# Kernel optimization log

Measured on AMD Instinct MI355X. Metric: run time of the kernel, lower is better.

The kernel has to match this reference:

```python
import jax, jax.numpy as jnp
import numpy as np

EPS = 1e-05  # matches tf entropy epsilon


def setup_inputs() -> dict:
    key = jax.random.key(0)
    k1, k2 = jax.random.split(key)
    encodings = jax.random.normal(k1, (8192, 64), dtype=jnp.float32)
    categorical = jax.random.uniform(k2, (8192, 25), dtype=jnp.float32)
    return {"encodings": encodings, "categorical": categorical, "k": 15}


def reference(encodings, categorical, k):
    B = encodings.shape[0]
    n_components = categorical.shape[1]
    k = min(k, B // 4)  # layer clamps k to batch_size // 4

    hard_groups = jnp.argmax(categorical, axis=1)           # [B] int
    max_groups = jnp.max(categorical, axis=1)               # [B]

    # Batched brute-force kNN. tf.norm's sqrt is monotonic, so the strict
    # comparison `dist < kth_dist` is identical on squared distances; working
    # in squared space avoids sqrt(0) issues and an extra pass.
    sq = jnp.sum(encodings * encodings, axis=1)             # [B]
    d2 = sq[:, None] + sq[None, :] - 2.0 * (encodings @ encodings.T)
    d2 = jnp.maximum(d2, 0.0)                               # [B, B]

    # (k+1)-smallest distances per row (0-indexed k, self-distance included,
    # matching tf.gather(tf.sort(distances), k)).
    neg_topk, _ = jax.lax.top_k(-d2, k + 1)                 # [B, k+1]
    kth = -neg_topk[:, k]                                   # [B] k-th smallest

    mask = (d2 < kth[:, None]).astype(jnp.float32)          # [B, B] strict <

    # Per-row label histogram over the neighborhood: counts[i,c] = #neighbors
    # of i in cluster c. Zero bins contribute 0 to -sum(b*log(b+eps)), same as
    # tf.bincount's variable-length output.
    onehot = jax.nn.one_hot(hard_groups, n_components, dtype=jnp.float32)
    counts = mask @ onehot                                  # [B, n_components]
    n_i = jnp.sum(counts, axis=-1, keepdims=True)           # [B, 1]
    bins = counts / jnp.maximum(n_i, 1.0)
    neighbourhood_entropy = -jnp.sum(bins * jnp.log(bins + EPS), axis=-1)  # [B]

    # Global cluster-size entropy + number of populated clusters.
    gcounts = jnp.sum(onehot, axis=0)                       # [n_components]
    gbins = gcounts / jnp.float32(B)
    cluster_size_entropy = -jnp.sum(gbins * jnp.log(gbins + EPS))
    n_populated = jnp.sum(gcounts > 0).astype(jnp.float32)

    return encodings, neighbourhood_entropy, cluster_size_entropy, n_populated, max_groups
```

## Files before the change

kernel.cpp:

```cpp
#include <hip/hip_runtime.h>
#include <math.h>

#define Bsz    8192
#define Dd     64
#define NC     25
#define RT     16
#define KCAP   16
#define EPSf   1e-5f

typedef short  short8  __attribute__((ext_vector_type(8)));
typedef float  floatx4 __attribute__((ext_vector_type(4)));


__device__ inline unsigned short f2bf(float x) {
    unsigned u = __float_as_uint(x);
    u += 0x7FFFu + ((u >> 16) & 1u);
    return (unsigned short)(u >> 16);
}
__device__ inline float bf2f(unsigned short h) { return __uint_as_float(((unsigned)h) << 16); }

__device__ inline void oesort8(unsigned* a) {
    #pragma unroll
    for (int p = 1; p < 8; p <<= 1) {
        #pragma unroll
        for (int k = p; k >= 1; k >>= 1) {
            #pragma unroll
            for (int j = (k & (p - 1)); j + k < 8; j += 2 * k) {
                #pragma unroll
                for (int i = 0; i < k; ++i) {
                    if (i + j + k < 8 &&
                        ((i + j) / (2 * p)) == ((i + j + k) / (2 * p))) {
                        unsigned x = a[i + j], y = a[i + j + k];
                        a[i + j]     = (x < y) ? x : y;
                        a[i + j + k] = (x < y) ? y : x;
                    }
                }
            }
        }
    }
}
__device__ inline void bclean16(unsigned* t) {
    #pragma unroll
    for (int j = 8; j > 0; j >>= 1)
        #pragma unroll
        for (int i = 0; i < 16; ++i) {
            int l = i ^ j;
            if (l > i) {
                unsigned x = t[i], y = t[l];
                t[i] = (x < y) ? x : y;
                t[l] = (x < y) ? y : x;
            }
        }
}
__device__ inline void bmerge16_8(unsigned* ls, const unsigned* c) {
    unsigned t[16];
    #pragma unroll
    for (int i = 0; i < 8; ++i) t[i] = ls[i];
    #pragma unroll
    for (int m = 0; m < 8; ++m) { unsigned x = ls[8 + m], y = c[7 - m]; t[8 + m] = (x < y) ? x : y; }
    bclean16(t);
    #pragma unroll
    for (int i = 0; i < 16; ++i) ls[i] = t[i];
}
__device__ inline void bmerge16(unsigned* ls, const unsigned* b) {
    unsigned t[16];
    #pragma unroll
    for (int i = 0; i < 16; ++i) { unsigned x = ls[i], y = b[15 - i]; t[i] = (x < y) ? x : y; }
    bclean16(t);
    #pragma unroll
    for (int i = 0; i < 16; ++i) ls[i] = t[i];
}
__device__ inline void bmerge16_shfl(unsigned* ls, int mask) {
    unsigned t[16];
    #pragma unroll
    for (int i = 0; i < 16; ++i) {
        unsigned pv = (unsigned)__shfl_xor((int)ls[15 - i], mask);
        unsigned x = ls[i];
        t[i] = (x < pv) ? x : pv;
    }
    bclean16(t);
    #pragma unroll
    for (int i = 0; i < 16; ++i) ls[i] = t[i];
}

__device__ __attribute__((always_inline)) inline void do_tile(
    const char* __restrict__ enc2, const unsigned* __restrict__ slab,
    int soff, int lane16, int quad4,
    const short8* bh, const short8* bl, float sqi, unsigned* cand)
{
    const char* base = enc2 + soff;
    short8 a0 = *(const short8*)(base + lane16);
    short8 a2 = *(const short8*)(base + lane16 + 2048);
    uint4  sv = *(const uint4*)(slab + (soff >> 8) + quad4);
    floatx4 acc = (floatx4){0.f, 0.f, 0.f, 0.f};
    acc = __builtin_amdgcn_mfma_f32_16x16x32_bf16(a0, bh[0], acc, 0, 0, 0);
    acc = __builtin_amdgcn_mfma_f32_16x16x32_bf16(a0, bl[0], acc, 0, 0, 0);
    acc = __builtin_amdgcn_mfma_f32_16x16x32_bf16(a2, bh[0], acc, 0, 0, 0);
    short8 a1 = *(const short8*)(base + lane16 + 1024);
    short8 a3 = *(const short8*)(base + lane16 + 3072);
    acc = __builtin_amdgcn_mfma_f32_16x16x32_bf16(a1, bh[1], acc, 0, 0, 0);
    acc = __builtin_amdgcn_mfma_f32_16x16x32_bf16(a1, bl[1], acc, 0, 0, 0);
    acc = __builtin_amdgcn_mfma_f32_16x16x32_bf16(a3, bh[1], acc, 0, 0, 0);

    unsigned s[4] = {sv.x, sv.y, sv.z, sv.w};
    #pragma unroll
    for (int r = 0; r < 4; ++r) {
        float d2 = fmaxf(sqi + __uint_as_float(s[r] & ~31u) + acc[r], 0.f);
        cand[r] = (__float_as_uint(d2) & ~31u) | (s[r] & 31u);
    }
}


__global__ __launch_bounds__(256) void pre_kernel(
    const float* __restrict__ enc, const float* __restrict__ cat,
    unsigned int* __restrict__ slab,
    char* __restrict__ enc1, char* __restrict__ enc2,
    float* __restrict__ out_max, float* __restrict__ out_enc)
{
    const int gid = blockIdx.x * 256 + threadIdx.x;
    const int p = gid >> 5, pr = gid & 31;

    float2 ev = ((const float2*)enc)[gid];
    ((float2*)out_enc)[gid] = ev;

    float s = ev.x * ev.x + ev.y * ev.y;
    #pragma unroll
    for (int m = 1; m < 32; m <<= 1) s += __shfl_xor(s, m, 32);

    {
        const int g = p >> 4, c15p = p & 15;
        const int d0 = 2 * pr, kh = d0 >> 5, q = (d0 >> 3) & 3, e0 = d0 & 7;
        const int base = g * 4096 + kh * 1024 + (q * 16 + c15p) * 16 + e0 * 2;
        unsigned short ha = f2bf(ev.x), hb = f2bf(ev.y);
        unsigned short la = f2bf(ev.x - bf2f(ha)), lb = f2bf(ev.y - bf2f(hb));
        *(unsigned*)(enc1 + base)        = (unsigned)ha | ((unsigned)hb << 16);
        *(unsigned*)(enc1 + base + 2048) = (unsigned)la | ((unsigned)lb << 16);
        float y0 = -2.f * ev.x, y1 = -2.f * ev.y;
        unsigned short hc = f2bf(y0), hd = f2bf(y1);
        unsigned short lc = f2bf(y0 - bf2f(hc)), ld = f2bf(y1 - bf2f(hd));
        *(unsigned*)(enc2 + base)        = (unsigned)hc | ((unsigned)hd << 16);
        *(unsigned*)(enc2 + base + 2048) = (unsigned)lc | ((unsigned)ld << 16);
    }
    float cv = (pr < NC) ? cat[p * NC + pr] : -1.f;
    int ci = pr;
    #pragma unroll
    for (int m = 1; m < 32; m <<= 1) {
        float ov = __shfl_xor(cv, m, 32);
        int   oi = __shfl_xor(ci, m, 32);
        if (ov > cv || (ov == cv && oi < ci)) { cv = ov; ci = oi; }
    }
    if (pr == 0) {
        out_max[p] = cv;
        slab[p] = (__float_as_uint(s) & ~31u) | (unsigned)ci;
    }
}

__global__ __launch_bounds__(1024, 8) void main_kernel(
    const char* __restrict__ enc1, const char* __restrict__ enc2,
    const unsigned int* __restrict__ slab, const int* __restrict__ kptr,
    float* __restrict__ out_ent, float* __restrict__ out_glob)
{
    __shared__ unsigned wl[16 * 16 * 17];
    __shared__ int cnt[32];

    const int tid  = threadIdx.x, bid = blockIdx.x;
    const int wv   = tid >> 6, lane = tid & 63;
    const int quad = (tid >> 4) & 3, c15 = tid & 15;
    const int rowbase = bid * RT;
    const int lane16 = lane * 16, quad4 = quad * 4;

    short8 bh[2], bl[2];
    {
        const char* ib = enc1 + (size_t)bid * 4096 + lane16;
        bh[0] = *(const short8*)(ib);
        bh[1] = *(const short8*)(ib + 1024);
        bl[0] = *(const short8*)(ib + 2048);
        bl[1] = *(const short8*)(ib + 3072);
    }
    const float sqi = __uint_as_float(slab[rowbase + c15] & ~31u);

    unsigned ls[KCAP];
    #pragma unroll
    for (int q = 0; q < KCAP; ++q) ls[q] = 0xFFFFFFFFu;

    const int wvoff = __builtin_amdgcn_readfirstlane(wv * 4096);

    #pragma unroll 1
    for (int m = 0; m < 16; ++m) {
        unsigned cand[8];
        const int soff = wvoff + m * 131072;
        do_tile(enc2, slab, soff,          lane16, quad4, bh, bl, sqi, cand);
        do_tile(enc2, slab, soff + 65536,  lane16, quad4, bh, bl, sqi, cand + 4);
        oesort8(cand);
        bmerge16_8(ls, cand);
    }

    if (bid == 0) {
        if (tid < 32) cnt[tid] = 0;
        __syncthreads();
        for (int i = tid; i < Bsz; i += 1024) atomicAdd(&cnt[slab[i] & 31u], 1);
        __syncthreads();
        if (tid == 0) {
            float gent = 0.f, npop = 0.f;
            for (int i = 0; i < NC; ++i) {
                int g = cnt[i];
                if (g > 0) {
                    npop += 1.f;
                    float gb = (float)g / (float)Bsz;
                    gent -= gb * logf(gb + EPSf);
                }
            }
            out_glob[0] = gent;
            out_glob[1] = npop;
        }
        __syncthreads();
    }

    bmerge16_shfl(ls, 16);
    bmerge16_shfl(ls, 32);
    if (quad == 0) {
        #pragma unroll
        for (int q = 0; q < KCAP; ++q) wl[(wv * 16 + c15) * 17 + q] = ls[q];
    }
    __syncthreads();
    if (wv == 0) {
        const int row = tid >> 2, sub = tid & 3;
        unsigned A[16], Bv[16];
        #pragma unroll
        for (int i = 0; i < 16; ++i) A[i]  = wl[((4 * sub)     * 16 + row) * 17 + i];
        #pragma unroll
        for (int i = 0; i < 16; ++i) Bv[i] = wl[((4 * sub + 1) * 16 + row) * 17 + i];
        bmerge16(A, Bv);
        #pragma unroll
        for (int i = 0; i < 16; ++i) Bv[i] = wl[((4 * sub + 2) * 16 + row) * 17 + i];
        bmerge16(A, Bv);
        #pragma unroll
        for (int i = 0; i < 16; ++i) Bv[i] = wl[((4 * sub + 3) * 16 + row) * 17 + i];
        bmerge16(A, Bv);
        bmerge16_shfl(A, 1);
        bmerge16_shfl(A, 2);

        int kk = kptr[0];
        if (kk > Bsz / 4) kk = Bsz / 4;
        if (kk > KCAP - 1) kk = KCAP - 1;

        unsigned kth = A[15];
        #pragma unroll
        for (int q = 0; q < 16; ++q) if (q == kk) kth = A[q];
        int nn = 0;
        #pragma unroll
        for (int t = 0; t < 15; ++t) nn += (t < kk && A[t] < kth) ? 1 : 0;

        float inv = 1.f / (float)((nn > 0) ? nn : 1);
        float part = 0.f;
        #pragma unroll
        for (int a4 = 0; a4 < 4; ++a4) {
            int a = sub + 4 * a4;
            if (a < nn) {
                int la = (int)(A[a] & 31u);
                int c = 0;
                #pragma unroll
                for (int b = 0; b < 15; ++b) c += (b < nn && (int)(A[b] & 31u) == la) ? 1 : 0;
                part -= inv * logf((float)c * inv + EPSf);
            }
        }
        part += __shfl_xor(part, 1);
        part += __shfl_xor(part, 2);
        if (sub == 0) out_ent[rowbase + row] = part;
    }
}

extern "C" void kernel_launch(void* const* d_in, const int* in_sizes, int n_in,
                              void* d_out, int out_size, void* d_ws, size_t ws_size,
                              hipStream_t stream)
{
    const float* enc  = (const float*)d_in[0];
    const float* cat  = (const float*)d_in[1];
    const int*   kptr = (const int*)d_in[2];
    float* out = (float*)d_out;

    unsigned int* slab = (unsigned int*)d_ws;
    char*         enc1 = (char*)d_ws + 32768;
    char*         enc2 = (char*)d_ws + 2129920;

    float* out_enc  = out;
    float* out_ent  = out + Bsz * Dd;
    float* out_glob = out + Bsz * Dd + Bsz;
    float* out_max  = out + Bsz * Dd + Bsz + 2;

    pre_kernel<<<1024, 256, 0, stream>>>(enc, cat, slab, enc1, enc2, out_max, out_enc);
    main_kernel<<<Bsz / RT, 1024, 0, stream>>>(enc1, enc2, slab, kptr, out_ent, out_glob);
}
```

Before: 124.7 us.

## Halve main kernel block size and software-pipeline tile loads with double-buffering

Cuts the main kNN kernel to 8 waves per block, so each wave now processes 32 column tiles instead of 16. Global loads for the next tile are issued ahead of the MFMAs on the current one through double-buffered register sets, with sched_barrier fences to keep that order. Candidates are now sorted in batches of 16 and merged with a full 16-wide bitonic merge, and the cross-wave LDS merge does fewer steps. The cost is higher register pressure from the live tile buffers, which may lower occupancy, and half as many threads per block.

```diff
diff --git a/kernel.cpp b/kernel.cpp
--- a/kernel.cpp
+++ b/kernel.cpp
@@ -7,6 +7,7 @@
 #define RT     16
 #define KCAP   16
 #define EPSf   1e-5f
+#define JMASK  2097151
 
 typedef short  short8  __attribute__((ext_vector_type(8)));
 typedef float  floatx4 __attribute__((ext_vector_type(4)));
@@ -19,16 +20,16 @@
 }
 __device__ inline float bf2f(unsigned short h) { return __uint_as_float(((unsigned)h) << 16); }
 
-__device__ inline void oesort8(unsigned* a) {
-    #pragma unroll
-    for (int p = 1; p < 8; p <<= 1) {
+__device__ inline void oesort16(unsigned* a) {
+    #pragma unroll
+    for (int p = 1; p < 16; p <<= 1) {
         #pragma unroll
         for (int k = p; k >= 1; k >>= 1) {
             #pragma unroll
-            for (int j = (k & (p - 1)); j + k < 8; j += 2 * k) {
+            for (int j = (k & (p - 1)); j + k < 16; j += 2 * k) {
                 #pragma unroll
                 for (int i = 0; i < k; ++i) {
-                    if (i + j + k < 8 &&
+                    if (i + j + k < 16 &&
                         ((i + j) / (2 * p)) == ((i + j + k) / (2 * p))) {
                         unsigned x = a[i + j], y = a[i + j + k];
                         a[i + j]     = (x < y) ? x : y;
@@ -52,16 +53,6 @@
             }
         }
 }
-__device__ inline void bmerge16_8(unsigned* ls, const unsigned* c) {
-    unsigned t[16];
-    #pragma unroll
-    for (int i = 0; i < 8; ++i) t[i] = ls[i];
-    #pragma unroll
-    for (int m = 0; m < 8; ++m) { unsigned x = ls[8 + m], y = c[7 - m]; t[8 + m] = (x < y) ? x : y; }
-    bclean16(t);
-    #pragma unroll
-    for (int i = 0; i < 16; ++i) ls[i] = t[i];
-}
 __device__ inline void bmerge16(unsigned* ls, const unsigned* b) {
     unsigned t[16];
     #pragma unroll
@@ -83,26 +74,32 @@
     for (int i = 0; i < 16; ++i) ls[i] = t[i];
 }
 
-__device__ __attribute__((always_inline)) inline void do_tile(
-    const char* __restrict__ enc2, const unsigned* __restrict__ slab,
-    int soff, int lane16, int quad4,
-    const short8* bh, const short8* bl, float sqi, unsigned* cand)
-{
-    const char* base = enc2 + soff;
-    short8 a0 = *(const short8*)(base + lane16);
-    short8 a2 = *(const short8*)(base + lane16 + 2048);
-    uint4  sv = *(const uint4*)(slab + (soff >> 8) + quad4);
+struct TileR { short8 a0, a1, a2, a3; uint4 sv; };
+
+__device__ __attribute__((always_inline)) inline void tile_load(
+    TileR& T, const char* __restrict__ enc2, const unsigned* __restrict__ slab,
+    int soff, int lane16, int quad4)
+{
+    const char* base = enc2 + soff + lane16;
+    T.a0 = *(const short8*)(base);
+    T.a1 = *(const short8*)(base + 1024);
+    T.a2 = *(const short8*)(base + 2048);
+    T.a3 = *(const short8*)(base + 3072);
+    T.sv = *(const uint4*)(slab + (soff >> 8) + quad4);
+}
+
+__device__ __attribute__((always_inline)) inline void tile_mfma(
+    const TileR& T, const short8* bh, const short8* bl, float sqi, unsigned* cand)
+{
     floatx4 acc = (floatx4){0.f, 0.f, 0.f, 0.f};
-    acc = __builtin_amdgcn_mfma_f32_16x16x32_bf16(a0, bh[0], acc, 0, 0, 0);
-    acc = __builtin_amdgcn_mfma_f32_16x16x32_bf16(a0, bl[0], acc, 0, 0, 0);
-    acc = __builtin_amdgcn_mfma_f32_16x16x32_bf16(a2, bh[0], acc, 0, 0, 0);
-    short8 a1 = *(const short8*)(base + lane16 + 1024);
-    short8 a3 = *(const short8*)(base + lane16 + 3072);
-    acc = __builtin_amdgcn_mfma_f32_16x16x32_bf16(a1, bh[1], acc, 0, 0, 0);
-    acc = __builtin_amdgcn_mfma_f32_16x16x32_bf16(a1, bl[1], acc, 0, 0, 0);
-    acc = __builtin_amdgcn_mfma_f32_16x16x32_bf16(a3, bh[1], acc, 0, 0, 0);
-
-    unsigned s[4] = {sv.x, sv.y, sv.z, sv.w};
+    acc = __builtin_amdgcn_mfma_f32_16x16x32_bf16(T.a0, bh[0], acc, 0, 0, 0);
+    acc = __builtin_amdgcn_mfma_f32_16x16x32_bf16(T.a0, bl[0], acc, 0, 0, 0);
+    acc = __builtin_amdgcn_mfma_f32_16x16x32_bf16(T.a2, bh[0], acc, 0, 0, 0);
+    acc = __builtin_amdgcn_mfma_f32_16x16x32_bf16(T.a1, bh[1], acc, 0, 0, 0);
+    acc = __builtin_amdgcn_mfma_f32_16x16x32_bf16(T.a1, bl[1], acc, 0, 0, 0);
+    acc = __builtin_amdgcn_mfma_f32_16x16x32_bf16(T.a3, bh[1], acc, 0, 0, 0);
+
+    unsigned s[4] = {T.sv.x, T.sv.y, T.sv.z, T.sv.w};
     #pragma unroll
     for (int r = 0; r < 4; ++r) {
         float d2 = fmaxf(sqi + __uint_as_float(s[r] & ~31u) + acc[r], 0.f);
@@ -155,12 +152,12 @@
     }
 }
 
-__global__ __launch_bounds__(1024, 8) void main_kernel(
+__global__ __launch_bounds__(512) void main_kernel(
     const char* __restrict__ enc1, const char* __restrict__ enc2,
     const unsigned int* __restrict__ slab, const int* __restrict__ kptr,
     float* __restrict__ out_ent, float* __restrict__ out_glob)
 {
-    __shared__ unsigned wl[16 * 16 * 17];
+    __shared__ unsigned wl[8 * 16 * 17];
     __shared__ int cnt[32];
 
     const int tid  = threadIdx.x, bid = blockIdx.x;
@@ -183,22 +180,47 @@
     #pragma unroll
     for (int q = 0; q < KCAP; ++q) ls[q] = 0xFFFFFFFFu;
 
-    const int wvoff = __builtin_amdgcn_readfirstlane(wv * 4096);
+    const int wvoff = wv * 4096;
+
+    TileR A0, A1, B0, B1;
+    tile_load(A0, enc2, slab, wvoff,          lane16, quad4);
+    tile_load(A1, enc2, slab, wvoff + 32768,  lane16, quad4);
 
     #pragma unroll 1
-    for (int m = 0; m < 16; ++m) {
-        unsigned cand[8];
-        const int soff = wvoff + m * 131072;
-        do_tile(enc2, slab, soff,          lane16, quad4, bh, bl, sqi, cand);
-        do_tile(enc2, slab, soff + 65536,  lane16, quad4, bh, bl, sqi, cand + 4);
-        oesort8(cand);
-        bmerge16_8(ls, cand);
+    for (int p = 0; p < 32; p += 2) {
+        unsigned cand[16];
+        {
+            const int o = (wvoff + (p + 1) * 65536) & JMASK;
+            tile_load(B0, enc2, slab, o, lane16, quad4);
+        }
+        __builtin_amdgcn_sched_barrier(0);
+        tile_mfma(A0, bh, bl, sqi, cand);
+        {
+            const int o = ((wvoff + (p + 1) * 65536) & JMASK) + 32768;
+            tile_load(B1, enc2, slab, o, lane16, quad4);
+        }
+        __builtin_amdgcn_sched_barrier(0);
+        tile_mfma(A1, bh, bl, sqi, cand + 4);
+        {
+            const int o = (wvoff + (p + 2) * 65536) & JMASK;
+            tile_load(A0, enc2, slab, o, lane16, quad4);
+        }
+        __builtin_amdgcn_sched_barrier(0);
+        tile_mfma(B0, bh, bl, sqi, cand + 8);
+        {
+            const int o = ((wvoff + (p + 2) * 65536) & JMASK) + 32768;
+            tile_load(A1, enc2, slab, o, lane16, quad4);
+        }
+        __builtin_amdgcn_sched_barrier(0);
+        tile_mfma(B1, bh, bl, sqi, cand + 12);
+        oesort16(cand);
+        bmerge16(ls, cand);
     }
 
     if (bid == 0) {
         if (tid < 32) cnt[tid] = 0;
         __syncthreads();
-        for (int i = tid; i < Bsz; i += 1024) atomicAdd(&cnt[slab[i] & 31u], 1);
+        for (int i = tid; i < Bsz; i += 512) atomicAdd(&cnt[slab[i] & 31u], 1);
         __syncthreads();
         if (tid == 0) {
             float gent = 0.f, npop = 0.f;
@@ -227,15 +249,9 @@
         const int row = tid >> 2, sub = tid & 3;
         unsigned A[16], Bv[16];
         #pragma unroll
-        for (int i = 0; i < 16; ++i) A[i]  = wl[((4 * sub)     * 16 + row) * 17 + i];
-        #pragma unroll
-        for (int i = 0; i < 16; ++i) Bv[i] = wl[((4 * sub + 1) * 16 + row) * 17 + i];
-        bmerge16(A, Bv);
-        #pragma unroll
-        for (int i = 0; i < 16; ++i) Bv[i] = wl[((4 * sub + 2) * 16 + row) * 17 + i];
-        bmerge16(A, Bv);
-        #pragma unroll
-        for (int i = 0; i < 16; ++i) Bv[i] = wl[((4 * sub + 3) * 16 + row) * 17 + i];
+        for (int i = 0; i < 16; ++i) A[i]  = wl[((2 * sub)     * 16 + row) * 17 + i];
+        #pragma unroll
+        for (int i = 0; i < 16; ++i) Bv[i] = wl[((2 * sub + 1) * 16 + row) * 17 + i];
         bmerge16(A, Bv);
         bmerge16_shfl(A, 1);
         bmerge16_shfl(A, 2);
@@ -289,5 +305,5 @@
     float* out_max  = out + Bsz * Dd + Bsz + 2;
 
     pre_kernel<<<1024, 256, 0, stream>>>(enc, cat, slab, enc1, enc2, out_max, out_enc);
-    main_kernel<<<Bsz / RT, 1024, 0, stream>>>(enc1, enc2, slab, kptr, out_ent, out_glob);
-}
+    main_kernel<<<Bsz / RT, 512, 0, stream>>>(enc1, enc2, slab, kptr, out_ent, out_glob);
+}
```

New measurement: 120.1 us. -3.7%, faster.
